# Optimization experiments

Measured on AMD Instinct MI355X. Metric: run time of the kernel, lower is better.

## Reference

```python
import jax, jax.numpy as jnp
import numpy as np

NV, NE = 4096, 8192
IN_V, OUT_V, IN_E = 128, 128, 64

def setup_inputs() -> dict:
    key = jax.random.key(0)
    ks = jax.random.split(key, 8)
    stdv = 1.0 / np.sqrt(OUT_V)
    return {
        "H_v": jax.random.normal(ks[0], (NV, IN_V), dtype=jnp.float32),
        "H_e": jax.random.normal(ks[1], (NE, IN_E), dtype=jnp.float32),
        "adj_e": jax.random.uniform(ks[2], (NE, NE), dtype=jnp.float32),
        "adj_v": jax.random.uniform(ks[3], (NV, NV), dtype=jnp.float32),
        "T": jax.random.uniform(ks[4], (NV, NE), dtype=jnp.float32),
        "weight": jax.random.uniform(ks[5], (IN_V, OUT_V), minval=-stdv, maxval=stdv, dtype=jnp.float32),
        "bias": jax.random.uniform(ks[6], (OUT_V,), minval=-stdv, maxval=stdv, dtype=jnp.float32),
        "p": jax.random.normal(ks[7], (1, IN_E), dtype=jnp.float32),
    }

def reference(H_v, H_e, adj_e, adj_v, T, weight, bias, p):
    # node_layer=True path of GraphConvolution.forward
    # diag_values = (H_e @ p.T).T[0]  -> [Ne]
    d = H_e @ p[0]                                   # [Ne]
    # T @ diag(d) @ T^T  ==  (T * d) @ T^T  (avoid materializing NxN diag)
    multiplier1 = (T * d[None, :]) @ T.T             # [Nv, Nv]
    # M1 = eye*1 + (1-eye)*multiplier1  -> set diagonal to 1
    idx = jnp.arange(multiplier1.shape[0])
    M1 = multiplier1.at[idx, idx].set(1.0)
    adjusted_A = M1 * adj_v                          # [Nv, Nv]
    output = adjusted_A @ (H_v @ weight) + bias      # [Nv, out_v]
    return (output, H_e)
```

## Files before the change

### kernel.cpp

```cpp
#include <hip/hip_runtime.h>
#include <cstdint>
#include <cstddef>

#define NV 4096
#define NE 8192
#define INV 128
#define OUTV 128
#define INE 64

#define BK 64
#define NT (NE / BK)
#define HALF_B 16384
#define LDS_BYTES (9 * HALF_B)

typedef __bf16 bf16x8 __attribute__((ext_vector_type(8)));
typedef float f32x4 __attribute__((ext_vector_type(4)));

__device__ __forceinline__ uint16_t f2bf(float x) {
  uint32_t u = __builtin_bit_cast(uint32_t, x);
  u += 0x7fff + ((u >> 16) & 1);
  return (uint16_t)(u >> 16);
}

__global__ void k_diag(const float* __restrict__ He, const float* __restrict__ p,
                       float* __restrict__ d) {
  int lane = threadIdx.x & 63;
  int wid = threadIdx.x >> 6;
  int row = blockIdx.x * 4 + wid;
  float v = He[(size_t)row * INE + lane] * p[lane];
#pragma unroll
  for (int off = 32; off; off >>= 1) v += __shfl_xor(v, off);
  if (lane == 0) d[row] = v;
}

__global__ void k_prep(const float4* __restrict__ T4, const float4* __restrict__ d4,
                       ushort4* __restrict__ A4, ushort4* __restrict__ B4) {
  const size_t total = (size_t)NV * NE / 4;
  size_t stride = (size_t)gridDim.x * blockDim.x;
  for (size_t i = (size_t)blockIdx.x * blockDim.x + threadIdx.x; i < total; i += stride) {
    float4 t = T4[i];
    float4 dv = d4[i & (NE / 4 - 1)];
    ushort4 a, b;
    b.x = f2bf(t.x); b.y = f2bf(t.y); b.z = f2bf(t.z); b.w = f2bf(t.w);
    a.x = f2bf(t.x * dv.x); a.y = f2bf(t.y * dv.y);
    a.z = f2bf(t.z * dv.z); a.w = f2bf(t.w * dv.w);
    A4[i] = a;
    B4[i] = b;
  }
}

__global__ void k_xw(const float* __restrict__ Hv, const float* __restrict__ W,
                     uint16_t* __restrict__ XT) {
  __shared__ float row[INV];
  int m = blockIdx.x;
  int n = threadIdx.x;
  row[n] = Hv[(size_t)m * INV + n];
  __syncthreads();
  float acc = 0.f;
#pragma unroll 8
  for (int k = 0; k < INV; ++k) acc += row[k] * W[k * OUTV + n];
  XT[(size_t)n * NV + m] = f2bf(acc);
}


__device__ __forceinline__ void gload16(const char* src, char* ldst) {
  __builtin_amdgcn_global_load_lds(
      (const __attribute__((address_space(1))) uint32_t*)src,
      (__attribute__((address_space(3))) uint32_t*)ldst, 16, 0, 0);
}

__global__ __launch_bounds__(512, 2) void k_gemm1(const uint16_t* __restrict__ A,
                                                  const uint16_t* __restrict__ B,
                                                  const float* __restrict__ adj_v,
                                                  uint16_t* __restrict__ adjA) {
  extern __shared__ char smem[];
  char* Aslot = smem;
  char* Bslot = smem + 5 * HALF_B;

  const int tid = threadIdx.x;
  const int lane = tid & 63, wid = tid >> 6;
  const int wr = wid >> 2, wc = wid & 3;
  const int lr = lane & 15, lk = lane >> 4;
  const int bcol0 = (wc & 1) * 64;

  int bid = blockIdx.x;
  int xcd = bid & 7, cid = bid >> 3;
  int bi = (xcd >> 1) * 4 + (cid >> 3);
  int bj = (xcd & 1) * 8 + (cid & 7);

  const int arow0 = bi * 256, brow0 = bj * 256;

  const int swz0 = ((lk) ^ (lr & 7)) << 4;
  const int swz1 = ((4 + lk) ^ (lr & 7)) << 4;
  const int pA0 = lr * 128 + swz0;
  const int pA1 = lr * 128 + swz1;
  const int pB0 = (bcol0 + lr) * 128 + swz0;
  const int pB1 = (bcol0 + lr) * 128 + swz1;

  const int srow = tid >> 3;
  const int sslot = (tid & 7) ^ (srow & 7);
  const int soff0 = srow * 16384 + sslot * 16;
  const int soff1 = soff0 + 64 * 16384;
  const char* Abase = (const char*)A + (size_t)arow0 * 16384;
  const char* Bbase = (const char*)B + (size_t)brow0 * 16384;
  const int ld0 = tid * 16;
  const int ld1 = tid * 16 + 8192;

  f32x4 acc[8][4] = {};
  bf16x8 af[4][2], af2[4][2], bfr[2][2], bfr2[2][2];

  {
    gload16(Abase + soff0, Aslot + ld0);
    gload16(Abase + soff1, Aslot + ld1);
    gload16(Abase + 2097152 + soff0, Aslot + HALF_B + ld0);
    gload16(Abase + 2097152 + soff1, Aslot + HALF_B + ld1);
    gload16(Bbase + soff0, Bslot + ld0);
    gload16(Bbase + soff1, Bslot + ld1);
    gload16(Bbase + 2097152 + soff0, Bslot + HALF_B + ld0);
    gload16(Bbase + 2097152 + soff1, Bslot + HALF_B + ld1);
    gload16(Abase + 128 + soff0, Aslot + 2 * HALF_B + ld0);
    gload16(Abase + 128 + soff1, Aslot + 2 * HALF_B + ld1);
  }
  asm volatile("s_waitcnt vmcnt(2)" ::: "memory");
  asm volatile("s_barrier" ::: "memory");

  int sA = 0;
  int sB = 0;
  for (int t = 0; t < NT; ++t) {
    const char* aB = Aslot + (((sA + wr) >= 5) ? (sA + wr - 5) : (sA + wr)) * HALF_B;
    const char* bB = Bslot + ((sB + (wc >> 1)) & 3) * HALF_B;
    const char* aK0 = aB + pA0;
    const char* aK1 = aB + pA1;
    const char* bK0 = bB + pB0;
    const char* bK1 = bB + pB1;
    const int k1 = (t + 1) * 128;
    const int k2 = (t + 2) * 128;

#pragma unroll
    for (int m = 0; m < 4; ++m) {
      af[m][0] = *(const bf16x8*)(aK0 + m * 2048);
      af[m][1] = *(const bf16x8*)(aK1 + m * 2048);
    }
#pragma unroll
    for (int n = 0; n < 2; ++n) {
      bfr[n][0] = *(const bf16x8*)(bK0 + n * 2048);
      bfr[n][1] = *(const bf16x8*)(bK1 + n * 2048);
    }
    if (t + 1 < NT) {
      int s1 = sA + 3; if (s1 >= 5) s1 -= 5;
      char* dA1 = Aslot + s1 * HALF_B;
      gload16(Abase + 2097152 + k1 + soff0, dA1 + ld0);
      gload16(Abase + 2097152 + k1 + soff1, dA1 + ld1);
      char* dB0 = Bslot + ((sB + 2) & 3) * HALF_B;
      gload16(Bbase + k1 + soff0, dB0 + ld0);
      gload16(Bbase + k1 + soff1, dB0 + ld1);
      char* dB1 = Bslot + ((sB + 3) & 3) * HALF_B;
      gload16(Bbase + 2097152 + k1 + soff0, dB1 + ld0);
      gload16(Bbase + 2097152 + k1 + soff1, dB1 + ld1);
    }
#pragma unroll
    for (int m = 0; m < 4; ++m)
#pragma unroll
      for (int n = 0; n < 2; ++n)
#pragma unroll
        for (int kk = 0; kk < 2; ++kk)
          acc[m][n] = __builtin_amdgcn_mfma_f32_16x16x32_bf16(af[m][kk], bfr[n][kk], acc[m][n], 0, 0, 0);

#pragma unroll
    for (int n = 0; n < 2; ++n) {
      bfr2[n][0] = *(const bf16x8*)(bK0 + 4096 + n * 2048);
      bfr2[n][1] = *(const bf16x8*)(bK1 + 4096 + n * 2048);
    }
    if (t + 2 < NT) {
      int s2 = sA + 4; if (s2 >= 5) s2 -= 5;
      char* dA0 = Aslot + s2 * HALF_B;
      gload16(Abase + k2 + soff0, dA0 + ld0);
      gload16(Abase + k2 + soff1, dA0 + ld1);
    }
#pragma unroll
    for (int m = 0; m < 4; ++m)
#pragma unroll
      for (int n = 0; n < 2; ++n)
#pragma unroll
        for (int kk = 0; kk < 2; ++kk)
          acc[m][2 + n] = __builtin_amdgcn_mfma_f32_16x16x32_bf16(af[m][kk], bfr2[n][kk], acc[m][2 + n], 0, 0, 0);

#pragma unroll
    for (int m = 0; m < 4; ++m) {
      af2[m][0] = *(const bf16x8*)(aK0 + 8192 + m * 2048);
      af2[m][1] = *(const bf16x8*)(aK1 + 8192 + m * 2048);
    }
#pragma unroll
    for (int m = 0; m < 4; ++m)
#pragma unroll
      for (int n = 0; n < 2; ++n)
#pragma unroll
        for (int kk = 0; kk < 2; ++kk)
          acc[4 + m][2 + n] = __builtin_amdgcn_mfma_f32_16x16x32_bf16(af2[m][kk], bfr2[n][kk], acc[4 + m][2 + n], 0, 0, 0);

#pragma unroll
    for (int m = 0; m < 4; ++m)
#pragma unroll
      for (int n = 0; n < 2; ++n)
#pragma unroll
        for (int kk = 0; kk < 2; ++kk)
          acc[4 + m][n] = __builtin_amdgcn_mfma_f32_16x16x32_bf16(af2[m][kk], bfr[n][kk], acc[4 + m][n], 0, 0, 0);

    if (t + 2 < NT) {
      asm volatile("s_waitcnt vmcnt(2)" ::: "memory");
    } else {
      asm volatile("s_waitcnt vmcnt(0)" ::: "memory");
    }
    asm volatile("s_barrier" ::: "memory");

    sA += 2; if (sA >= 5) sA -= 5;
    sB ^= 2;
  }

#pragma unroll
  for (int m = 0; m < 8; ++m) {
    int grow0 = bi * 256 + wr * 128 + m * 16 + lk * 4;
#pragma unroll
    for (int n = 0; n < 4; ++n) {
      int gcol = bj * 256 + wc * 64 + n * 16 + lr;
#pragma unroll
      for (int r = 0; r < 4; ++r) {
        int grow = grow0 + r;
        float v = acc[m][n][r];
        if (grow == gcol) v = 1.0f;
        adjA[(size_t)grow * NV + gcol] = f2bf(v * adj_v[(size_t)grow * NV + gcol]);
      }
    }
  }
}

__global__ __launch_bounds__(256) void k_gemm2p(const uint16_t* __restrict__ A,
                                                const uint16_t* __restrict__ B,
                                                float* __restrict__ part) {
  __shared__ __align__(16) uint16_t As[128 * 32];
  __shared__ __align__(16) uint16_t Bs[128 * 32];
  const int tid = threadIdx.x;
  const int wid = tid >> 6, lane = tid & 63;
  const int wr = wid >> 1, wc = wid & 1;
  const int ks = blockIdx.x & 7;
  const int bi = blockIdx.x >> 3;
  const int lr = lane & 15, lk = lane >> 4;

  f32x4 acc[4][4] = {};

  for (int kt = ks * 16; kt < ks * 16 + 16; ++kt) {
#pragma unroll
    for (int i = 0; i < 2; ++i) {
      int o = (wid * 2 + i) * 1024 + lane * 16;
      int row = o >> 6, kb = o & 63;
      const char* ga = (const char*)A + ((size_t)(bi * 128 + row) * NV + kt * 32) * 2 + kb;
      const char* gb = (const char*)B + ((size_t)row * NV + kt * 32) * 2 + kb;
      __builtin_amdgcn_global_load_lds(
          (const __attribute__((address_space(1))) uint32_t*)ga,
          (__attribute__((address_space(3))) uint32_t*)((char*)As + (wid * 2 + i) * 1024),
          16, 0, 0);
      __builtin_amdgcn_global_load_lds(
          (const __attribute__((address_space(1))) uint32_t*)gb,
          (__attribute__((address_space(3))) uint32_t*)((char*)Bs + (wid * 2 + i) * 1024),
          16, 0, 0);
    }
    __syncthreads();
    bf16x8 af[4], bfr[4];
#pragma unroll
    for (int m = 0; m < 4; ++m)
      af[m] = *(const bf16x8*)&As[(wr * 64 + m * 16 + lr) * 32 + lk * 8];
#pragma unroll
    for (int n = 0; n < 4; ++n)
      bfr[n] = *(const bf16x8*)&Bs[(wc * 64 + n * 16 + lr) * 32 + lk * 8];
#pragma unroll
    for (int m = 0; m < 4; ++m)
#pragma unroll
      for (int n = 0; n < 4; ++n)
        acc[m][n] = __builtin_amdgcn_mfma_f32_16x16x32_bf16(af[m], bfr[n], acc[m][n], 0, 0, 0);
    __syncthreads();
  }

  float* my = part + (size_t)ks * NV * OUTV;
#pragma unroll
  for (int m = 0; m < 4; ++m) {
    int grow0 = bi * 128 + wr * 64 + m * 16 + lk * 4;
#pragma unroll
    for (int n = 0; n < 4; ++n) {
      int gcol = wc * 64 + n * 16 + lr;
#pragma unroll
      for (int r = 0; r < 4; ++r)
        my[(size_t)(grow0 + r) * OUTV + gcol] = acc[m][n][r];
    }
  }
}

__global__ void k_gemm2r(const float4* __restrict__ part, const float* __restrict__ bias,
                         float4* __restrict__ out) {
  int i = blockIdx.x * 256 + threadIdx.x;
  float4 s = part[i];
#pragma unroll
  for (int ks = 1; ks < 8; ++ks) {
    float4 q = part[(size_t)ks * (NV * OUTV / 4) + i];
    s.x += q.x; s.y += q.y; s.z += q.z; s.w += q.w;
  }
  float4 b = ((const float4*)bias)[i & 31];
  s.x += b.x; s.y += b.y; s.z += b.z; s.w += b.w;
  out[i] = s;
}

extern "C" void kernel_launch(void* const* d_in, const int* in_sizes, int n_in,
                              void* d_out, int out_size, void* d_ws, size_t ws_size,
                              hipStream_t stream) {
  const float* Hv = (const float*)d_in[0];
  const float* He = (const float*)d_in[1];
  const float* adj_v = (const float*)d_in[3];
  const float* T = (const float*)d_in[4];
  const float* W = (const float*)d_in[5];
  const float* bias = (const float*)d_in[6];
  const float* p = (const float*)d_in[7];
  float* out = (float*)d_out;

  char* ws = (char*)d_ws;
  float* dvec = (float*)ws;
  uint16_t* XT = (uint16_t*)(ws + 32768);
  uint16_t* Abf = (uint16_t*)(ws + 32768 + (1u << 20));
  uint16_t* Bbf = Abf + (size_t)NV * NE;
  uint16_t* adjA = Bbf + (size_t)NV * NE;
  float* part = (float*)Abf;

  static int lds_attr_set = 0;
  if (!lds_attr_set) {
    hipFuncSetAttribute((const void*)k_gemm1,
                        hipFuncAttributeMaxDynamicSharedMemorySize, LDS_BYTES);
    lds_attr_set = 1;
  }

  k_diag<<<NE / 4, 256, 0, stream>>>(He, p, dvec);
  k_prep<<<2048, 256, 0, stream>>>((const float4*)T, (const float4*)dvec,
                                   (ushort4*)Abf, (ushort4*)Bbf);
  k_xw<<<NV, INV, 0, stream>>>(Hv, W, XT);
  k_gemm1<<<256, 512, LDS_BYTES, stream>>>(Abf, Bbf, adj_v, adjA);
  k_gemm2p<<<256, 256, 0, stream>>>(adjA, XT, part);
  k_gemm2r<<<NV * OUTV / 4 / 256, 256, 0, stream>>>((const float4*)part, bias, (float4*)out);
  hipMemcpyAsync(out + (size_t)NV * OUTV, He, (size_t)NE * INE * sizeof(float),
                 hipMemcpyDeviceToDevice, stream);
}
```

Measured before the change: 287.8 us.

## Exploit symmetry of T·diag(d)·Tᵀ with split-K upper-triangle GEMM and reduction

The Gram-like product (T*d)@Tᵀ is symmetric, so only the 136 upper-triangular 256x256 tile pairs are computed. Each pair's K dimension is split three ways to fill the GPU, and the partials are written as bf16. A new reduction kernel sums the three partials, sets the diagonal to one, multiplies by adj_v, and writes both the tile and its transpose through LDS. This roughly halves GEMM1 MFMA work, at the cost of extra partial-buffer traffic, a separate reduce pass, and added bf16 rounding of the partials. The new path runs only if the workspace is large enough; otherwise the old kernel is used.

```diff
diff --git a/kernel.cpp b/kernel.cpp
--- a/kernel.cpp
+++ b/kernel.cpp
@@ -12,6 +12,9 @@
 #define NT (NE / BK)
 #define HALF_B 16384
 #define LDS_BYTES (9 * HALF_B)
+#define NPAIR 136
+#define NKS 3
+#define NBLK (NPAIR * NKS)
 
 typedef __bf16 bf16x8 __attribute__((ext_vector_type(8)));
 typedef float f32x4 __attribute__((ext_vector_type(4)));
@@ -20,6 +23,10 @@
   uint32_t u = __builtin_bit_cast(uint32_t, x);
   u += 0x7fff + ((u >> 16) & 1);
   return (uint16_t)(u >> 16);
+}
+__device__ __forceinline__ float bf2f(uint16_t u) {
+  uint32_t v = ((uint32_t)u) << 16;
+  return __builtin_bit_cast(float, v);
 }
 
 __global__ void k_diag(const float* __restrict__ He, const float* __restrict__ p,
@@ -62,11 +69,215 @@
   XT[(size_t)n * NV + m] = f2bf(acc);
 }
 
-
 __device__ __forceinline__ void gload16(const char* src, char* ldst) {
   __builtin_amdgcn_global_load_lds(
       (const __attribute__((address_space(1))) uint32_t*)src,
       (__attribute__((address_space(3))) uint32_t*)ldst, 16, 0, 0);
+}
+
+__global__ __launch_bounds__(512, 2) void k_gemm1s(const uint16_t* __restrict__ A,
+                                                   const uint16_t* __restrict__ B,
+                                                   uint16_t* __restrict__ part) {
+  extern __shared__ char smem[];
+  char* Aslot = smem;
+  char* Bslot = smem + 5 * HALF_B;
+
+  const int tid = threadIdx.x;
+  const int lane = tid & 63, wid = tid >> 6;
+  const int wr = wid >> 2, wc = wid & 3;
+  const int lr = lane & 15, lk = lane >> 4;
+  const int bcol0 = (wc & 1) * 64;
+
+  const int idx = blockIdx.x;
+  const int ks = idx / NPAIR;
+  int qq = idx - ks * NPAIR;
+  int a = 0;
+  while (qq >= 16 - a) { qq -= 16 - a; ++a; }
+  const int b = a + qq;
+
+  const int k0t = ks * 43;
+  const int nt = (ks < 2) ? 43 : 42;
+  const int kb0 = k0t * 128;
+
+  const int swz0 = ((lk) ^ (lr & 7)) << 4;
+  const int swz1 = ((4 + lk) ^ (lr & 7)) << 4;
+  const int pA0 = lr * 128 + swz0;
+  const int pA1 = lr * 128 + swz1;
+  const int pB0 = (bcol0 + lr) * 128 + swz0;
+  const int pB1 = (bcol0 + lr) * 128 + swz1;
+
+  const int srow = tid >> 3;
+  const int sslot = (tid & 7) ^ (srow & 7);
+  const int soff0 = srow * 16384 + sslot * 16;
+  const int soff1 = soff0 + 64 * 16384;
+  const char* Abase = (const char*)A + (size_t)(a * 256) * 16384;
+  const char* Bbase = (const char*)B + (size_t)(b * 256) * 16384;
+  const int ld0 = tid * 16;
+  const int ld1 = tid * 16 + 8192;
+
+  f32x4 acc[8][4] = {};
+  bf16x8 af[4][2], af2[4][2], bfr[2][2], bfr2[2][2];
+
+  gload16(Abase + kb0 + soff0, Aslot + ld0);
+  gload16(Abase + kb0 + soff1, Aslot + ld1);
+  gload16(Abase + 2097152 + kb0 + soff0, Aslot + HALF_B + ld0);
+  gload16(Abase + 2097152 + kb0 + soff1, Aslot + HALF_B + ld1);
+  gload16(Bbase + kb0 + soff0, Bslot + ld0);
+  gload16(Bbase + kb0 + soff1, Bslot + ld1);
+  gload16(Bbase + 2097152 + kb0 + soff0, Bslot + HALF_B + ld0);
+  gload16(Bbase + 2097152 + kb0 + soff1, Bslot + HALF_B + ld1);
+  gload16(Abase + kb0 + 128 + soff0, Aslot + 2 * HALF_B + ld0);
+  gload16(Abase + kb0 + 128 + soff1, Aslot + 2 * HALF_B + ld1);
+  asm volatile("s_waitcnt vmcnt(2)" ::: "memory");
+  asm volatile("s_barrier" ::: "memory");
+
+  int sA = 0;
+  int sB = 0;
+  for (int t = 0; t < nt; ++t) {
+    const char* aB = Aslot + (((sA + wr) >= 5) ? (sA + wr - 5) : (sA + wr)) * HALF_B;
+    const char* bB = Bslot + ((sB + (wc >> 1)) & 3) * HALF_B;
+    const char* aK0 = aB + pA0;
+    const char* aK1 = aB + pA1;
+    const char* bK0 = bB + pB0;
+    const char* bK1 = bB + pB1;
+    const int k1 = kb0 + (t + 1) * 128;
+    const int k2 = kb0 + (t + 2) * 128;
+
+#pragma unroll
+    for (int m = 0; m < 4; ++m) {
+      af[m][0] = *(const bf16x8*)(aK0 + m * 2048);
+      af[m][1] = *(const bf16x8*)(aK1 + m * 2048);
+    }
+#pragma unroll
+    for (int n = 0; n < 2; ++n) {
+      bfr[n][0] = *(const bf16x8*)(bK0 + n * 2048);
+      bfr[n][1] = *(const bf16x8*)(bK1 + n * 2048);
+    }
+    if (t + 1 < nt) {
+      int s1 = sA + 3; if (s1 >= 5) s1 -= 5;
+      char* dA1 = Aslot + s1 * HALF_B;
+      gload16(Abase + 2097152 + k1 + soff0, dA1 + ld0);
+      gload16(Abase + 2097152 + k1 + soff1, dA1 + ld1);
+      char* dB0 = Bslot + ((sB + 2) & 3) * HALF_B;
+      gload16(Bbase + k1 + soff0, dB0 + ld0);
+      gload16(Bbase + k1 + soff1, dB0 + ld1);
+      char* dB1 = Bslot + ((sB + 3) & 3) * HALF_B;
+      gload16(Bbase + 2097152 + k1 + soff0, dB1 + ld0);
+      gload16(Bbase + 2097152 + k1 + soff1, dB1 + ld1);
+    }
+#pragma unroll
+    for (int m = 0; m < 4; ++m)
+#pragma unroll
+      for (int n = 0; n < 2; ++n)
+#pragma unroll
+        for (int kk = 0; kk < 2; ++kk)
+          acc[m][n] = __builtin_amdgcn_mfma_f32_16x16x32_bf16(af[m][kk], bfr[n][kk], acc[m][n], 0, 0, 0);
+
+#pragma unroll
+    for (int n = 0; n < 2; ++n) {
+      bfr2[n][0] = *(const bf16x8*)(bK0 + 4096 + n * 2048);
+      bfr2[n][1] = *(const bf16x8*)(bK1 + 4096 + n * 2048);
+    }
+    if (t + 2 < nt) {
+      int s2 = sA + 4; if (s2 >= 5) s2 -= 5;
+      char* dA0 = Aslot + s2 * HALF_B;
+      gload16(Abase + k2 + soff0, dA0 + ld0);
+      gload16(Abase + k2 + soff1, dA0 + ld1);
+    }
+#pragma unroll
+    for (int m = 0; m < 4; ++m)
+#pragma unroll
+      for (int n = 0; n < 2; ++n)
+#pragma unroll
+        for (int kk = 0; kk < 2; ++kk)
+          acc[m][2 + n] = __builtin_amdgcn_mfma_f32_16x16x32_bf16(af[m][kk], bfr2[n][kk], acc[m][2 + n], 0, 0, 0);
+
+#pragma unroll
+    for (int m = 0; m < 4; ++m) {
+      af2[m][0] = *(const bf16x8*)(aK0 + 8192 + m * 2048);
+      af2[m][1] = *(const bf16x8*)(aK1 + 8192 + m * 2048);
+    }
+#pragma unroll
+    for (int m = 0; m < 4; ++m)
+#pragma unroll
+      for (int n = 0; n < 2; ++n)
+#pragma unroll
+        for (int kk = 0; kk < 2; ++kk)
+          acc[4 + m][2 + n] = __builtin_amdgcn_mfma_f32_16x16x32_bf16(af2[m][kk], bfr2[n][kk], acc[4 + m][2 + n], 0, 0, 0);
+
+#pragma unroll
+    for (int m = 0; m < 4; ++m)
+#pragma unroll
+      for (int n = 0; n < 2; ++n)
+#pragma unroll
+        for (int kk = 0; kk < 2; ++kk)
+          acc[4 + m][n] = __builtin_amdgcn_mfma_f32_16x16x32_bf16(af2[m][kk], bfr[n][kk], acc[4 + m][n], 0, 0, 0);
+
+    if (t + 2 < nt) {
+      asm volatile("s_waitcnt vmcnt(2)" ::: "memory");
+    } else {
+      asm volatile("s_waitcnt vmcnt(0)" ::: "memory");
+    }
+    asm volatile("s_barrier" ::: "memory");
+
+    sA += 2; if (sA >= 5) sA -= 5;
+    sB ^= 2;
+  }
+
+  uint16_t* myp = part + (size_t)idx * 65536;
+#pragma unroll
+  for (int m = 0; m < 8; ++m) {
+    int rowb = wr * 128 + m * 16 + lk * 4;
+#pragma unroll
+    for (int n = 0; n < 4; ++n) {
+      int col = wc * 64 + n * 16 + lr;
+#pragma unroll
+      for (int r = 0; r < 4; ++r)
+        myp[(rowb + r) * 256 + col] = f2bf(acc[m][n][r]);
+    }
+  }
+}
+
+__global__ __launch_bounds__(256) void k_m1red(const uint16_t* __restrict__ part,
+                                               const float* __restrict__ adj_v,
+                                               uint16_t* __restrict__ adjA) {
+  __shared__ float ls[64][65];
+  int tq = blockIdx.x;
+  int SI = 0;
+  while (tq >= 64 - SI) { tq -= 64 - SI; ++SI; }
+  int SJ = SI + tq;
+  const int R0 = SI * 64, C0 = SJ * 64;
+  const int a = SI >> 2, b = SJ >> 2;
+  const int q = 16 * a - (a * (a - 1)) / 2 + (b - a);
+  const uint16_t* p0 = part + (size_t)q * 65536 + (size_t)(R0 & 255) * 256 + (C0 & 255);
+
+  const int tx = threadIdx.x & 63, ty = threadIdx.x >> 6;
+  float vals[16];
+#pragma unroll
+  for (int yy = 0; yy < 16; ++yy) {
+    int x = ty * 16 + yy;
+    float s = bf2f(p0[x * 256 + tx]) + bf2f(p0[(size_t)NPAIR * 65536 + x * 256 + tx]) +
+              bf2f(p0[(size_t)(2 * NPAIR) * 65536 + x * 256 + tx]);
+    vals[yy] = s;
+    ls[x][tx] = s;
+  }
+  __syncthreads();
+#pragma unroll
+  for (int yy = 0; yy < 16; ++yy) {
+    int x = ty * 16 + yy;
+    int gr = R0 + x, gc = C0 + tx;
+    float v = (gr == gc) ? 1.0f : vals[yy];
+    adjA[(size_t)gr * NV + gc] = f2bf(v * adj_v[(size_t)gr * NV + gc]);
+  }
+  if (SI != SJ) {
+#pragma unroll
+    for (int yy = 0; yy < 16; ++yy) {
+      int x = ty * 16 + yy;
+      float tv = ls[tx][x];
+      int gr = C0 + x, gc = R0 + tx;
+      adjA[(size_t)gr * NV + gc] = f2bf(tv * adj_v[(size_t)gr * NV + gc]);
+    }
+  }
 }
 
 __global__ __launch_bounds__(512, 2) void k_gemm1(const uint16_t* __restrict__ A,
@@ -88,8 +299,6 @@
   int bi = (xcd >> 1) * 4 + (cid >> 3);
   int bj = (xcd & 1) * 8 + (cid & 7);
 
-  const int arow0 = bi * 256, brow0 = bj * 256;
-
   const int swz0 = ((lk) ^ (lr & 7)) << 4;
   const int swz1 = ((4 + lk) ^ (lr & 7)) << 4;
   const int pA0 = lr * 128 + swz0;
@@ -101,31 +310,28 @@
   const int sslot = (tid & 7) ^ (srow & 7);
   const int soff0 = srow * 16384 + sslot * 16;
   const int soff1 = soff0 + 64 * 16384;
-  const char* Abase = (const char*)A + (size_t)arow0 * 16384;
-  const char* Bbase = (const char*)B + (size_t)brow0 * 16384;
+  const char* Abase = (const char*)A + (size_t)(bi * 256) * 16384;
+  const char* Bbase = (const char*)B + (size_t)(bj * 256) * 16384;
   const int ld0 = tid * 16;
   const int ld1 = tid * 16 + 8192;
 
   f32x4 acc[8][4] = {};
   bf16x8 af[4][2], af2[4][2], bfr[2][2], bfr2[2][2];
 
-  {
-    gload16(Abase + soff0, Aslot + ld0);
-    gload16(Abase + soff1, Aslot + ld1);
-    gload16(Abase + 2097152 + soff0, Aslot + HALF_B + ld0);
-    gload16(Abase + 2097152 + soff1, Aslot + HALF_B + ld1);
-    gload16(Bbase + soff0, Bslot + ld0);
-    gload16(Bbase + soff1, Bslot + ld1);
-    gload16(Bbase + 2097152 + soff0, Bslot + HALF_B + ld0);
-    gload16(Bbase + 2097152 + soff1, Bslot + HALF_B + ld1);
-    gload16(Abase + 128 + soff0, Aslot + 2 * HALF_B + ld0);
-    gload16(Abase + 128 + soff1, Aslot + 2 * HALF_B + ld1);
-  }
+  gload16(Abase + soff0, Aslot + ld0);
+  gload16(Abase + soff1, Aslot + ld1);
+  gload16(Abase + 2097152 + soff0, Aslot + HALF_B + ld0);
+  gload16(Abase + 2097152 + soff1, Aslot + HALF_B + ld1);
+  gload16(Bbase + soff0, Bslot + ld0);
+  gload16(Bbase + soff1, Bslot + ld1);
+  gload16(Bbase + 2097152 + soff0, Bslot + HALF_B + ld0);
+  gload16(Bbase + 2097152 + soff1, Bslot + HALF_B + ld1);
+  gload16(Abase + 128 + soff0, Aslot + 2 * HALF_B + ld0);
+  gload16(Abase + 128 + soff1, Aslot + 2 * HALF_B + ld1);
   asm volatile("s_waitcnt vmcnt(2)" ::: "memory");
   asm volatile("s_barrier" ::: "memory");
 
-  int sA = 0;
-  int sB = 0;
+  int sA = 0, sB = 0;
   for (int t = 0; t < NT; ++t) {
     const char* aB = Aslot + (((sA + wr) >= 5) ? (sA + wr - 5) : (sA + wr)) * HALF_B;
     const char* bB = Bslot + ((sB + (wc >> 1)) & 3) * HALF_B;
@@ -325,13 +531,16 @@
   uint16_t* XT = (uint16_t*)(ws + 32768);
   uint16_t* Abf = (uint16_t*)(ws + 32768 + (1u << 20));
   uint16_t* Bbf = Abf + (size_t)NV * NE;
-  uint16_t* adjA = Bbf + (size_t)NV * NE;
-  float* part = (float*)Abf;
+
+  const size_t base = 32768 + (1u << 20) + 2 * (size_t)NV * NE * 2;
+  const size_t need_sym = base + (size_t)NBLK * 65536 * 2;
 
   static int lds_attr_set = 0;
   if (!lds_attr_set) {
     hipFuncSetAttribute((const void*)k_gemm1,
                         hipFuncAttributeMaxDynamicSharedMemorySize, LDS_BYTES);
+    hipFuncSetAttribute((const void*)k_gemm1s,
+                        hipFuncAttributeMaxDynamicSharedMemorySize, LDS_BYTES);
     lds_attr_set = 1;
   }
 
@@ -339,9 +548,23 @@
   k_prep<<<2048, 256, 0, stream>>>((const float4*)T, (const float4*)dvec,
                                    (ushort4*)Abf, (ushort4*)Bbf);
   k_xw<<<NV, INV, 0, stream>>>(Hv, W, XT);
-  k_gemm1<<<256, 512, LDS_BYTES, stream>>>(Abf, Bbf, adj_v, adjA);
-  k_gemm2p<<<256, 256, 0, stream>>>(adjA, XT, part);
-  k_gemm2r<<<NV * OUTV / 4 / 256, 256, 0, stream>>>((const float4*)part, bias, (float4*)out);
+
+  if (ws_size >= need_sym) {
+    uint16_t* part16 = (uint16_t*)(ws + base);
+    uint16_t* adjA = Abf;
+    float* part2 = (float*)Bbf;
+    k_gemm1s<<<NBLK, 512, LDS_BYTES, stream>>>(Abf, Bbf, part16);
+    k_m1red<<<2080, 256, 0, stream>>>(part16, adj_v, adjA);
+    k_gemm2p<<<256, 256, 0, stream>>>(adjA, XT, part2);
+    k_gemm2r<<<NV * OUTV / 4 / 256, 256, 0, stream>>>((const float4*)part2, bias, (float4*)out);
+  } else {
+    uint16_t* adjA = Bbf + (size_t)NV * NE;
+    float* part2 = (float*)Abf;
+    k_gemm1<<<256, 512, LDS_BYTES, stream>>>(Abf, Bbf, adj_v, adjA);
+    k_gemm2p<<<256, 256, 0, stream>>>(adjA, XT, part2);
+    k_gemm2r<<<NV * OUTV / 4 / 256, 256, 0, stream>>>((const float4*)part2, bias, (float4*)out);
+  }
+
   hipMemcpyAsync(out + (size_t)NV * OUTV, He, (size_t)NE * INE * sizeof(float),
                  hipMemcpyDeviceToDevice, stream);
 }
```

Measured after the change: 269.2 us. 1.07x faster.
